# Performance work log

Hardware: AMD Instinct MI355X
Metric: run time of the kernel (lower is better)

## Reference

```python
import jax, jax.numpy as jnp
import numpy as np

HEADS = 8
DIM_HEAD = 64
QUERY_DIM = 1024
CONTEXT_DIM = 768
INNER = HEADS * DIM_HEAD  # 512


def setup_inputs() -> dict:
    key = jax.random.key(0)
    ks = jax.random.split(key, 7)
    B, Sq, Skv = 4, 4096, 1024
    x = jax.random.normal(ks[0], (B, Sq, QUERY_DIM), dtype=jnp.float32)
    context = jax.random.normal(ks[1], (B, Skv, CONTEXT_DIM), dtype=jnp.float32)
    # nn.Linear(in, out) weights stored as [out, in]; we use [in, out] for x @ W
    Wq = jax.random.normal(ks[2], (QUERY_DIM, INNER), dtype=jnp.float32) * (QUERY_DIM ** -0.5)
    Wk = jax.random.normal(ks[3], (CONTEXT_DIM, INNER), dtype=jnp.float32) * (CONTEXT_DIM ** -0.5)
    Wv = jax.random.normal(ks[4], (CONTEXT_DIM, INNER), dtype=jnp.float32) * (CONTEXT_DIM ** -0.5)
    Wo = jax.random.normal(ks[5], (INNER, QUERY_DIM), dtype=jnp.float32) * (INNER ** -0.5)
    bo = jax.random.normal(ks[6], (QUERY_DIM,), dtype=jnp.float32) * 0.01
    return {"x": x, "context": context, "Wq": Wq, "Wk": Wk, "Wv": Wv, "Wo": Wo, "bo": bo}


def reference(x, context, Wq, Wk, Wv, Wo, bo):
    B, Sq, _ = x.shape
    h, d = HEADS, DIM_HEAD
    scale = d ** -0.5
    # project and split heads: [B, S, h*d] -> [B, h, S, d]
    q = (x @ Wq).reshape(B, Sq, h, d).transpose(0, 2, 1, 3)
    k = (context @ Wk).reshape(B, -1, h, d).transpose(0, 2, 1, 3)
    v = (context @ Wv).reshape(B, -1, h, d).transpose(0, 2, 1, 3)
    # the torch chunked loop is exactly full softmax attention (softmax is row-wise)
    scores = jnp.einsum('bhid,bhjd->bhij', q, k) * scale
    attn = jax.nn.softmax(scores, axis=-1)
    out = jnp.einsum('bhij,bhjd->bhid', attn, v)  # [B, h, Sq, d]
    out = out.transpose(0, 2, 1, 3).reshape(B, Sq, h * d)
    return out @ Wo + bo
```

## Files before the change

### kernel.cpp

```cpp
#include <hip/hip_runtime.h>

#define SQ 4096
#define SKV 1024
#define BATCH 4
#define NH 8
#define DH 64
#define QD 1024
#define CD 768
#define INNER 512

typedef _Float16 half8 __attribute__((ext_vector_type(8)));
typedef _Float16 half4v __attribute__((ext_vector_type(4)));
typedef float floatx4 __attribute__((ext_vector_type(4)));
typedef float f32x16 __attribute__((ext_vector_type(16)));
typedef unsigned int uint4v __attribute__((ext_vector_type(4)));

#define MFMA16(a, b, c) __builtin_amdgcn_mfma_f32_16x16x32_f16(a, b, c, 0, 0, 0)
#define MFMA32(a, b, c) __builtin_amdgcn_mfma_f32_32x32x16_f16(a, b, c, 0, 0, 0)

#define PLSWAP(a, b) asm("v_permlane32_swap_b32 %0, %1" : "+v"(a), "+v"(b))

#define GLD16(gptr, lptr)                                                            \
  __builtin_amdgcn_global_load_lds(                                                  \
      (const __attribute__((address_space(1))) unsigned int*)(const void*)(gptr),    \
      (__attribute__((address_space(3))) unsigned int*)(void*)(lptr), 16, 0, 0)

__global__ __launch_bounds__(256) void transpose_all(const float* __restrict__ Wq,
                                                     const float* __restrict__ Wk,
                                                     const float* __restrict__ Wv,
                                                     const float* __restrict__ Wo,
                                                     _Float16* __restrict__ wqt,
                                                     _Float16* __restrict__ wkvt,
                                                     _Float16* __restrict__ wot) {
  __shared__ float tile[32][33];
  const int z = blockIdx.z;
  const float* src; _Float16* dst; int R, C;
  if (z == 0)      { src = Wq; dst = wqt;                        R = QD;    C = INNER; }
  else if (z == 1) { src = Wk; dst = wkvt;                       R = CD;    C = INNER; }
  else if (z == 2) { src = Wv; dst = wkvt + (size_t)INNER * CD;  R = CD;    C = INNER; }
  else             { src = Wo; dst = wot;                        R = INNER; C = QD;   }
  const int c0 = blockIdx.x * 32, r0 = blockIdx.y * 32;
  if (c0 >= C || r0 >= R) return;
  const int tx = threadIdx.x & 31, ty = threadIdx.x >> 5;
#pragma unroll
  for (int i = 0; i < 32; i += 8)
    tile[ty + i][tx] = src[(size_t)(r0 + ty + i) * C + c0 + tx];
  __syncthreads();
#pragma unroll
  for (int i = 0; i < 32; i += 8)
    dst[(size_t)(c0 + ty + i) * R + r0 + tx] = (_Float16)tile[tx][ty + i];
}

template <int MODE, int AF32>
__global__ __launch_bounds__(256) void gemm128(const void* __restrict__ Aany,
                                               const _Float16* __restrict__ Bt,
                                               void* __restrict__ Cout,
                                               void* __restrict__ Cout2,
                                               const float* __restrict__ bias,
                                               int M, int N, int K) {
  __shared__ char AsRaw[AF32 ? 128 * 32 * 4 : 128 * 32 * 2];
  __shared__ _Float16 Bs[128 * 32];
  float* As32 = (float*)AsRaw;
  _Float16* As16 = (_Float16*)AsRaw;

  const int tid = threadIdx.x;
  const int wave = tid >> 6, lane = tid & 63;
  const int quad = lane >> 4, l16 = lane & 15;
  const int wm = (wave >> 1) * 64, wn = (wave & 1) * 64;
  const size_t n0 = (size_t)blockIdx.x * 128, m0 = (size_t)blockIdx.y * 128;

  floatx4 acc[4][4] = {};

  const float* a32g = (const float*)Aany + (m0 + (tid >> 3)) * (size_t)K + (tid & 7) * 4;
  const _Float16* a16g = (const _Float16*)Aany + (m0 + (tid >> 2)) * (size_t)K + (tid & 3) * 8;
  const _Float16* bg = Bt + (n0 + (tid >> 2)) * (size_t)K + (tid & 3) * 8;

  for (int k0 = 0; k0 < K; k0 += 32) {
    __syncthreads();
    if (AF32) {
#pragma unroll
      for (int j = 0; j < 4; ++j)
        GLD16(a32g + k0 + (size_t)j * 32 * K, As32 + tid * 4 + j * 1024);
    } else {
#pragma unroll
      for (int j = 0; j < 2; ++j)
        GLD16(a16g + k0 + (size_t)j * 64 * K, As16 + tid * 8 + j * 2048);
    }
#pragma unroll
    for (int j = 0; j < 2; ++j)
      GLD16(bg + k0 + (size_t)j * 64 * K, Bs + tid * 8 + j * 2048);
    __syncthreads();

    half8 af[4], bf[4];
#pragma unroll
    for (int mt = 0; mt < 4; ++mt) {
      const int row = wm + mt * 16 + l16;
      if (AF32) {
        floatx4 x0 = *(const floatx4*)(As32 + row * 32 + quad * 8);
        floatx4 x1 = *(const floatx4*)(As32 + row * 32 + quad * 8 + 4);
        half8 t;
#pragma unroll
        for (int i = 0; i < 4; ++i) { t[i] = (_Float16)x0[i]; t[4 + i] = (_Float16)x1[i]; }
        af[mt] = t;
      } else {
        af[mt] = *(const half8*)(As16 + row * 32 + quad * 8);
      }
    }
#pragma unroll
    for (int nt = 0; nt < 4; ++nt)
      bf[nt] = *(const half8*)(Bs + (wn + nt * 16 + l16) * 32 + quad * 8);
#pragma unroll
    for (int mt = 0; mt < 4; ++mt)
#pragma unroll
      for (int nt = 0; nt < 4; ++nt)
        acc[mt][nt] = MFMA16(af[mt], bf[nt], acc[mt][nt]);
  }

  if (MODE == 0 || MODE == 3) {
    _Float16* C = (_Float16*)Cout;
    const float sc = (MODE == 3) ? 0.125f * 1.44269504088896f : 1.0f;
#pragma unroll
    for (int mt = 0; mt < 4; ++mt) {
      const size_t row = m0 + wm + mt * 16 + quad * 4;
#pragma unroll
      for (int nt = 0; nt < 4; ++nt) {
        const size_t col = n0 + wn + nt * 16 + l16;
#pragma unroll
        for (int r = 0; r < 4; ++r)
          C[(row + r) * N + col] = (_Float16)(acc[mt][nt][r] * sc);
      }
    }
  } else if (MODE == 4) {
    if (n0 < INNER) {
      _Float16* C = (_Float16*)Cout;
#pragma unroll
      for (int mt = 0; mt < 4; ++mt) {
        const size_t row = m0 + wm + mt * 16 + quad * 4;
#pragma unroll
        for (int nt = 0; nt < 4; ++nt) {
          const size_t col = n0 + wn + nt * 16 + l16;
#pragma unroll
          for (int r = 0; r < 4; ++r)
            C[(row + r) * INNER + col] = (_Float16)acc[mt][nt][r];
        }
      }
    } else {
      _Float16* C = (_Float16*)Cout2;
      const int b = (int)(m0 >> 10);
#pragma unroll
      for (int mt = 0; mt < 4; ++mt) {
        const int kvb = (int)(m0 & 1023) + wm + mt * 16 + quad * 4;
#pragma unroll
        for (int nt = 0; nt < 4; ++nt) {
          const int col = (int)(n0 - INNER + wn + nt * 16 + l16);
          const int h = col >> 6, d = col & 63;
          half4v pk;
#pragma unroll
          for (int r = 0; r < 4; ++r) pk[r] = (_Float16)acc[mt][nt][r];
          *(half4v*)(C + (size_t)((b * NH + h) * DH + d) * SKV + kvb) = pk;
        }
      }
    }
  } else {
    float* C = (float*)Cout;
#pragma unroll
    for (int mt = 0; mt < 4; ++mt) {
      const size_t row = m0 + wm + mt * 16 + quad * 4;
#pragma unroll
      for (int nt = 0; nt < 4; ++nt) {
        const size_t col = n0 + wn + nt * 16 + l16;
        const float bb = bias[col];
#pragma unroll
        for (int r = 0; r < 4; ++r)
          C[(row + r) * N + col] = acc[mt][nt][r] + bb;
      }
    }
  }
}

__global__ __launch_bounds__(256, 3) void flash_attn7(const _Float16* __restrict__ Q,
                                                      const _Float16* __restrict__ Kp,
                                                      const _Float16* __restrict__ Vt,
                                                      _Float16* __restrict__ O) {
  __shared__ _Float16 Ksb[2 * 64 * 64];
  __shared__ _Float16 Vsb[2 * 64 * 64];
  const int tid = threadIdx.x;
  const int wave = tid >> 6, lane = tid & 63;
  const int l31 = lane & 31, hi = lane >> 5, x7 = lane & 7;

  const int flat = blockIdx.x;
  const int nf = (flat & 7) * 128 + (flat >> 3);
  const int qblk = nf & 31, bh = nf >> 5;
  const int b = bh >> 3, h = bh & 7;

  const size_t qrow0 = (size_t)b * SQ + qblk * 128 + wave * 32;
  const _Float16* qptr = Q + qrow0 * INNER + h * DH;
  const _Float16* kbase = Kp + (size_t)b * SKV * INNER + h * DH;
  const _Float16* vbase = Vt + (size_t)bh * DH * SKV;

  const int kr = tid >> 3;
  const int kb = (tid & 7) ^ (kr & 7);
  const _Float16* kg = kbase + (size_t)kr * INNER + kb * 8;
  const _Float16* vg = vbase + (size_t)kr * SKV + kb * 8;

#define STAGE_KV(bi, tt)                                                        \
  do {                                                                          \
    _Float16* _kl = Ksb + (bi) * 4096 + tid * 8;                                \
    _Float16* _vl = Vsb + (bi) * 4096 + tid * 8;                                \
    GLD16(kg + (size_t)((tt) * 64) * INNER, _kl);                               \
    GLD16(kg + (size_t)((tt) * 64 + 32) * INNER, _kl + 2048);                   \
    GLD16(vg + (tt) * 64, _vl);                                                 \
    GLD16(vg + (size_t)32 * SKV + (tt) * 64, _vl + 2048);                       \
  } while (0)

  half8 aq[4];
#pragma unroll
  for (int i = 0; i < 4; ++i)
    aq[i] = *(const half8*)(qptr + (size_t)l31 * INNER + i * 16 + hi * 8);

  int koff[4], voffB[4];
#pragma unroll
  for (int i = 0; i < 4; ++i)
    koff[i] = l31 * 64 + (((i * 2 + hi) ^ x7) << 3);
#pragma unroll
  for (int j = 0; j < 4; ++j)
    voffB[j] = l31 * 64 + (((j * 2 + hi) ^ x7) << 3);

  half8 ones;
#pragma unroll
  for (int j = 0; j < 8; ++j) ones[j] = (_Float16)1.0f;

  f32x16 o0 = {}, o1 = {}, osum = {};

  STAGE_KV(0, 0);

  for (int t = 0; t < SKV / 64; ++t) {
    __syncthreads();
    if (t < SKV / 64 - 1) STAGE_KV((t + 1) & 1, t + 1);
    const _Float16* ks = Ksb + (t & 1) * 4096;
    const _Float16* vs = Vsb + (t & 1) * 4096;

#pragma unroll
    for (int c2 = 0; c2 < 2; ++c2) {
      half8 ak[4];
#pragma unroll
      for (int i = 0; i < 4; ++i)
        ak[i] = *(const half8*)(ks + c2 * 2048 + koff[i]);

      f32x16 st = {};
#pragma unroll
      for (int i = 0; i < 4; ++i) st = MFMA32(ak[i], aq[i], st);

      unsigned w[8];
#pragma unroll
      for (int j = 0; j < 8; ++j) {
        float plo = __builtin_exp2f(st[2 * j]);
        float phi = __builtin_exp2f(st[2 * j + 1]);
        w[j] = __builtin_bit_cast(unsigned, __builtin_amdgcn_cvt_pkrtz(plo, phi));
      }
      PLSWAP(w[0], w[2]);
      PLSWAP(w[1], w[3]);
      PLSWAP(w[4], w[6]);
      PLSWAP(w[5], w[7]);
      uint4v u0 = {w[0], w[1], w[2], w[3]};
      uint4v u1 = {w[4], w[5], w[6], w[7]};
      half8 A0 = __builtin_bit_cast(half8, u0);
      half8 A1 = __builtin_bit_cast(half8, u1);

      osum = MFMA32(A0, ones, osum);
      osum = MFMA32(A1, ones, osum);

      {
        half8 bv00 = *(const half8*)(vs + 0 * 2048 + voffB[c2 * 2 + 0]);
        half8 bv10 = *(const half8*)(vs + 1 * 2048 + voffB[c2 * 2 + 0]);
        o0 = MFMA32(A0, bv00, o0);
        o1 = MFMA32(A0, bv10, o1);
        half8 bv01 = *(const half8*)(vs + 0 * 2048 + voffB[c2 * 2 + 1]);
        half8 bv11 = *(const half8*)(vs + 1 * 2048 + voffB[c2 * 2 + 1]);
        o0 = MFMA32(A1, bv01, o0);
        o1 = MFMA32(A1, bv11, o1);
      }
    }
  }

  float inv16[16];
#pragma unroll
  for (int r = 0; r < 16; ++r) inv16[r] = 1.0f / osum[r];

  _Float16* op = O + qrow0 * INNER + h * DH;
#pragma unroll
  for (int r = 0; r < 16; ++r) {
    const int q = (r & 3) + 8 * (r >> 2) + 4 * hi;
    op[(size_t)q * INNER + l31] = (_Float16)(o0[r] * inv16[r]);
    op[(size_t)q * INNER + 32 + l31] = (_Float16)(o1[r] * inv16[r]);
  }
#undef STAGE_KV
}

extern "C" void kernel_launch(void* const* d_in, const int* in_sizes, int n_in,
                              void* d_out, int out_size, void* d_ws, size_t ws_size,
                              hipStream_t stream) {
  const float* x   = (const float*)d_in[0];
  const float* ctx = (const float*)d_in[1];
  const float* Wq  = (const float*)d_in[2];
  const float* Wk  = (const float*)d_in[3];
  const float* Wv  = (const float*)d_in[4];
  const float* Wo  = (const float*)d_in[5];
  const float* bo  = (const float*)d_in[6];
  float* out = (float*)d_out;

  _Float16* ws = (_Float16*)d_ws;
  _Float16* wqt  = ws;
  _Float16* wkvt = wqt + (size_t)INNER * QD;
  _Float16* wot  = wkvt + (size_t)2 * INNER * CD;
  _Float16* qh   = wot + (size_t)QD * INNER;
  _Float16* kh   = qh + (size_t)BATCH * SQ * INNER;
  _Float16* vth  = kh + (size_t)BATCH * SKV * INNER;
  _Float16* aoh  = vth + (size_t)BATCH * SKV * INNER;

  transpose_all<<<dim3(32, 32, 4), 256, 0, stream>>>(Wq, Wk, Wv, Wo, wqt, wkvt, wot);

  gemm128<3, 1><<<dim3(INNER / 128, BATCH * SQ / 128), 256, 0, stream>>>(
      (const void*)x, wqt, (void*)qh, nullptr, nullptr, BATCH * SQ, INNER, QD);
  gemm128<4, 1><<<dim3(2 * INNER / 128, BATCH * SKV / 128), 256, 0, stream>>>(
      (const void*)ctx, wkvt, (void*)kh, (void*)vth, nullptr, BATCH * SKV, 2 * INNER, CD);

  flash_attn7<<<dim3(BATCH * NH * SQ / 128), 256, 0, stream>>>(qh, kh, vth, aoh);

  gemm128<2, 0><<<dim3(QD / 128, BATCH * SQ / 128), 256, 0, stream>>>(
      (const void*)aoh, wot, (void*)out, nullptr, bo, BATCH * SQ, QD, INNER);
}
```

Before: 288.1 us.

## Pre-cast inputs to fp16 and fuse Q and KV projections into one launch

A new elementwise kernel casts x and context to fp16 up front, so the projection GEMMs load fp16 A tiles instead of fp32 tiles converted in registers. The Q projection and the KV projection become one interleaved grid of 768 blocks, which cuts a launch and improves occupancy across the smaller KV GEMM. The attention output buffer reuses the xh workspace region. The change adds a full extra read and write pass over the activations in exchange for half-size A loads and smaller shared memory in the GEMMs.

```diff
diff --git a/kernel.cpp b/kernel.cpp
--- a/kernel.cpp
+++ b/kernel.cpp
@@ -24,6 +24,25 @@
   __builtin_amdgcn_global_load_lds(                                                  \
       (const __attribute__((address_space(1))) unsigned int*)(const void*)(gptr),    \
       (__attribute__((address_space(3))) unsigned int*)(void*)(lptr), 16, 0, 0)
+
+__global__ __launch_bounds__(256) void cast_f2h(const float* __restrict__ x,
+                                                const float* __restrict__ ctx,
+                                                _Float16* __restrict__ xh,
+                                                _Float16* __restrict__ ctxh) {
+  const size_t NX = (size_t)BATCH * SQ * QD;
+  size_t i = ((size_t)blockIdx.x * 256 + threadIdx.x) * 8;
+  const float* s;
+  _Float16* d;
+  size_t off;
+  if (i < NX) { s = x; d = xh; off = i; }
+  else        { s = ctx; d = ctxh; off = i - NX; }
+  floatx4 a = *(const floatx4*)(s + off);
+  floatx4 b = *(const floatx4*)(s + off + 4);
+  half8 h;
+#pragma unroll
+  for (int j = 0; j < 4; ++j) { h[j] = (_Float16)a[j]; h[4 + j] = (_Float16)b[j]; }
+  *(half8*)(d + off) = h;
+}
 
 __global__ __launch_bounds__(256) void transpose_all(const float* __restrict__ Wq,
                                                      const float* __restrict__ Wk,
@@ -51,41 +70,30 @@
     dst[(size_t)(c0 + ty + i) * R + r0 + tx] = (_Float16)tile[tx][ty + i];
 }
 
-template <int MODE, int AF32>
-__global__ __launch_bounds__(256) void gemm128(const void* __restrict__ Aany,
-                                               const _Float16* __restrict__ Bt,
-                                               void* __restrict__ Cout,
-                                               void* __restrict__ Cout2,
-                                               const float* __restrict__ bias,
-                                               int M, int N, int K) {
-  __shared__ char AsRaw[AF32 ? 128 * 32 * 4 : 128 * 32 * 2];
-  __shared__ _Float16 Bs[128 * 32];
-  float* As32 = (float*)AsRaw;
-  _Float16* As16 = (_Float16*)AsRaw;
-
+template <int MODE>
+__device__ __forceinline__ void gemm_body(const _Float16* __restrict__ A,
+                                          const _Float16* __restrict__ Bt,
+                                          void* __restrict__ Cout,
+                                          void* __restrict__ Cout2,
+                                          const float* __restrict__ bias,
+                                          int M, int N, int K, int bx, int by,
+                                          _Float16* As16, _Float16* Bs) {
   const int tid = threadIdx.x;
   const int wave = tid >> 6, lane = tid & 63;
   const int quad = lane >> 4, l16 = lane & 15;
   const int wm = (wave >> 1) * 64, wn = (wave & 1) * 64;
-  const size_t n0 = (size_t)blockIdx.x * 128, m0 = (size_t)blockIdx.y * 128;
+  const size_t n0 = (size_t)bx * 128, m0 = (size_t)by * 128;
 
   floatx4 acc[4][4] = {};
 
-  const float* a32g = (const float*)Aany + (m0 + (tid >> 3)) * (size_t)K + (tid & 7) * 4;
-  const _Float16* a16g = (const _Float16*)Aany + (m0 + (tid >> 2)) * (size_t)K + (tid & 3) * 8;
+  const _Float16* ag = A + (m0 + (tid >> 2)) * (size_t)K + (tid & 3) * 8;
   const _Float16* bg = Bt + (n0 + (tid >> 2)) * (size_t)K + (tid & 3) * 8;
 
   for (int k0 = 0; k0 < K; k0 += 32) {
     __syncthreads();
-    if (AF32) {
-#pragma unroll
-      for (int j = 0; j < 4; ++j)
-        GLD16(a32g + k0 + (size_t)j * 32 * K, As32 + tid * 4 + j * 1024);
-    } else {
-#pragma unroll
-      for (int j = 0; j < 2; ++j)
-        GLD16(a16g + k0 + (size_t)j * 64 * K, As16 + tid * 8 + j * 2048);
-    }
+#pragma unroll
+    for (int j = 0; j < 2; ++j)
+      GLD16(ag + k0 + (size_t)j * 64 * K, As16 + tid * 8 + j * 2048);
 #pragma unroll
     for (int j = 0; j < 2; ++j)
       GLD16(bg + k0 + (size_t)j * 64 * K, Bs + tid * 8 + j * 2048);
@@ -93,19 +101,8 @@
 
     half8 af[4], bf[4];
 #pragma unroll
-    for (int mt = 0; mt < 4; ++mt) {
-      const int row = wm + mt * 16 + l16;
-      if (AF32) {
-        floatx4 x0 = *(const floatx4*)(As32 + row * 32 + quad * 8);
-        floatx4 x1 = *(const floatx4*)(As32 + row * 32 + quad * 8 + 4);
-        half8 t;
-#pragma unroll
-        for (int i = 0; i < 4; ++i) { t[i] = (_Float16)x0[i]; t[4 + i] = (_Float16)x1[i]; }
-        af[mt] = t;
-      } else {
-        af[mt] = *(const half8*)(As16 + row * 32 + quad * 8);
-      }
-    }
+    for (int mt = 0; mt < 4; ++mt)
+      af[mt] = *(const half8*)(As16 + (wm + mt * 16 + l16) * 32 + quad * 8);
 #pragma unroll
     for (int nt = 0; nt < 4; ++nt)
       bf[nt] = *(const half8*)(Bs + (wn + nt * 16 + l16) * 32 + quad * 8);
@@ -116,9 +113,9 @@
         acc[mt][nt] = MFMA16(af[mt], bf[nt], acc[mt][nt]);
   }
 
-  if (MODE == 0 || MODE == 3) {
+  if (MODE == 3) {
     _Float16* C = (_Float16*)Cout;
-    const float sc = (MODE == 3) ? 0.125f * 1.44269504088896f : 1.0f;
+    const float sc = 0.125f * 1.44269504088896f;
 #pragma unroll
     for (int mt = 0; mt < 4; ++mt) {
       const size_t row = m0 + wm + mt * 16 + quad * 4;
@@ -176,6 +173,37 @@
       }
     }
   }
+}
+
+__global__ __launch_bounds__(256) void proj_fused(const _Float16* __restrict__ xh,
+                                                  const _Float16* __restrict__ ctxh,
+                                                  const _Float16* __restrict__ wqt,
+                                                  const _Float16* __restrict__ wkvt,
+                                                  _Float16* __restrict__ qh,
+                                                  _Float16* __restrict__ kh,
+                                                  _Float16* __restrict__ vth) {
+  __shared__ _Float16 As16[128 * 32];
+  __shared__ _Float16 Bs[128 * 32];
+  const int id = blockIdx.x;
+  const int seg = id % 3, base = id / 3;
+  if (seg == 2) {
+    gemm_body<4>(ctxh, wkvt, kh, vth, nullptr, BATCH * SKV, 2 * INNER, CD,
+                 base & 7, base >> 3, As16, Bs);
+  } else {
+    const int q = base * 2 + seg;
+    gemm_body<3>(xh, wqt, qh, nullptr, nullptr, BATCH * SQ, INNER, QD,
+                 q & 3, q >> 2, As16, Bs);
+  }
+}
+
+__global__ __launch_bounds__(256) void gemm_out(const _Float16* __restrict__ A,
+                                                const _Float16* __restrict__ Bt,
+                                                float* __restrict__ Cout,
+                                                const float* __restrict__ bias) {
+  __shared__ _Float16 As16[128 * 32];
+  __shared__ _Float16 Bs[128 * 32];
+  gemm_body<2>(A, Bt, Cout, nullptr, bias, BATCH * SQ, QD, INNER,
+               blockIdx.x, blockIdx.y, As16, Bs);
 }
 
 __global__ __launch_bounds__(256, 3) void flash_attn7(const _Float16* __restrict__ Q,
@@ -309,24 +337,27 @@
   const float* bo  = (const float*)d_in[6];
   float* out = (float*)d_out;
 
+  const size_t NX = (size_t)BATCH * SQ * QD;
+  const size_t NC = (size_t)BATCH * SKV * CD;
+
   _Float16* ws = (_Float16*)d_ws;
-  _Float16* wqt  = ws;
+  _Float16* xh   = ws;
+  _Float16* ctxh = xh + NX;
+  _Float16* wqt  = ctxh + NC;
   _Float16* wkvt = wqt + (size_t)INNER * QD;
   _Float16* wot  = wkvt + (size_t)2 * INNER * CD;
   _Float16* qh   = wot + (size_t)QD * INNER;
   _Float16* kh   = qh + (size_t)BATCH * SQ * INNER;
   _Float16* vth  = kh + (size_t)BATCH * SKV * INNER;
-  _Float16* aoh  = vth + (size_t)BATCH * SKV * INNER;
+  _Float16* aoh  = xh;
+
+  cast_f2h<<<dim3((unsigned)((NX + NC) / 2048)), 256, 0, stream>>>(x, ctx, xh, ctxh);
 
   transpose_all<<<dim3(32, 32, 4), 256, 0, stream>>>(Wq, Wk, Wv, Wo, wqt, wkvt, wot);
 
-  gemm128<3, 1><<<dim3(INNER / 128, BATCH * SQ / 128), 256, 0, stream>>>(
-      (const void*)x, wqt, (void*)qh, nullptr, nullptr, BATCH * SQ, INNER, QD);
-  gemm128<4, 1><<<dim3(2 * INNER / 128, BATCH * SKV / 128), 256, 0, stream>>>(
-      (const void*)ctx, wkvt, (void*)kh, (void*)vth, nullptr, BATCH * SKV, 2 * INNER, CD);
+  proj_fused<<<dim3(768), 256, 0, stream>>>(xh, ctxh, wqt, wkvt, qh, kh, vth);
 
   flash_attn7<<<dim3(BATCH * NH * SQ / 128), 256, 0, stream>>>(qh, kh, vth, aoh);
 
-  gemm128<2, 0><<<dim3(QD / 128, BATCH * SQ / 128), 256, 0, stream>>>(
-      (const void*)aoh, wot, (void*)out, nullptr, bo, BATCH * SQ, QD, INNER);
-}
+  gemm_out<<<dim3(QD / 128, BATCH * SQ / 128), 256, 0, stream>>>(aoh, wot, out, bo);
+}
```

After: 270.6 us. -6.1%, faster.
